# Kernel tuning notes

Hardware: AMD Instinct MI355X
Metric: run time of the kernel (lower is better)

Reference implementation:

```python
import jax, jax.numpy as jnp
import numpy as np

V, D, T, B, MS, WIN, EOS = 10000, 256, 128, 8, 4, 1, 4
S = MS + 1          # decoder segment length (y_input0 + MAX_SEGMENT tokens)
HRATE = 0.1
LOGINF = 1e6


def setup_inputs() -> dict:
    key = jax.random.key(0)
    ks = jax.random.split(key, 17)
    s = lambda i, shape: (jax.random.normal(ks[i], shape, jnp.float32) * 0.05)
    return dict(
        x_ids=jax.random.randint(ks[0], (B, T + 2 * WIN), 0, V),
        lens=jnp.full((B,), T, dtype=jnp.int32),
        emb=s(1, (V, D)),
        y_start=s(2, (1, D)),
        cell_Wi=s(3, (4 * D, D)), cell_Wh=s(4, (4 * D, D)), cell_b=s(5, (4 * D,)),
        yin0_W=s(6, (D, D)), yin0_b=s(7, (D,)),
        hlin_W=s(8, (2 * D, D)), hlin_b=s(9, (2 * D,)),
        l0_Wi=s(10, (4 * D, D)), l0_Wh=s(11, (4 * D, D)), l0_b=s(12, (4 * D,)),
        l1_Wi=s(13, (4 * D, D)), l1_Wh=s(14, (4 * D, D)), l1_b=s(15, (4 * D,)),
        out_b=s(16, (V,)),
    )


def _cell(x, h, c, Wi, Wh, b):
    # torch LSTM gate order: i, f, g, o
    g = x @ Wi.T + h @ Wh.T + b
    i, f, gg, o = jnp.split(g, 4, axis=-1)
    c2 = jax.nn.sigmoid(f) * c + jax.nn.sigmoid(i) * jnp.tanh(gg)
    return jax.nn.sigmoid(o) * jnp.tanh(c2), c2


def reference(x_ids, lens, emb, y_start, cell_Wi, cell_Wh, cell_b,
              yin0_W, yin0_b, hlin_W, hlin_b,
              l0_Wi, l0_Wh, l0_b, l1_Wi, l1_Wh, l1_b, out_b):
    y = x_ids[:, WIN:-WIN]                     # [B, T] target ids
    x = emb[y]                                 # [B, T, D]

    # --- encoder LSTMCell scan over j_start (state persists across schedule) ---
    seq = jnp.concatenate(
        [jnp.broadcast_to(y_start, (B, D))[None], jnp.transpose(x, (1, 0, 2))[:-1]], 0)  # [T,B,D]
    z = jnp.zeros((B, D), x.dtype)
    def enc_step(carry, xt):
        h, c = carry
        h2, c2 = _cell(xt, h, c, cell_Wi, cell_Wh, cell_b)
        return (h2, c2), h2
    _, h_seq = jax.lax.scan(enc_step, (z, z), seq)        # [T, B, D]

    drop_h = HRATE * h_seq
    y_in0 = drop_h @ yin0_W.T + yin0_b                    # [T, B, D]
    h0_all = jnp.tanh(drop_h @ hlin_W.T + hlin_b).reshape(T, B, 2, D)  # per-layer init h

    # --- build decoder inputs [T, B, S, D]: (y_input0, x[j_start:j_start+MS]) ---
    xp = jnp.pad(x, ((0, 0), (0, MS), (0, 0)))            # zero-pad time (causal => pads don't affect valid outputs)
    pos = jnp.arange(T)[:, None] + jnp.arange(MS)[None, :]           # [T, MS]
    seg_x = jnp.transpose(xp[:, pos], (1, 0, 2, 3))       # [T, B, MS, D]
    seg = jnp.concatenate([y_in0[:, :, None, :], seg_x], axis=2)     # [T, B, S, D]

    # --- 2-layer LSTM decoder, vmapped over j_start ---
    def decode(seg_t, h_init):                            # seg_t [B,S,D], h_init [B,2,D]
        def step(carry, xt):
            (h0, c0), (h1, c1) = carry
            h0n, c0n = _cell(xt, h0, c0, l0_Wi, l0_Wh, l0_b)
            h1n, c1n = _cell(h0n, h1, c1, l1_Wi, l1_Wh, l1_b)
            return ((h0n, c0n), (h1n, c1n)), h1n
        init = ((h_init[:, 0], z), (h_init[:, 1], z))
        _, hs = jax.lax.scan(step, init, jnp.transpose(seg_t, (1, 0, 2)))
        return jnp.transpose(hs, (1, 0, 2))               # [B, S, D]
    dec_h = jax.vmap(decode)(seg, h0_all)                 # [T, B, S, D]

    # --- tied output projection + log-softmax (only needed gathers kept) ---
    logits = jnp.einsum('tbsd,vd->tbsv', dec_h, emb) + out_b         # [T,B,S,V]
    logZ = jax.nn.logsumexp(logits, axis=-1)                          # [T,B,S]

    tgt = jnp.transpose(y[:, jnp.clip(pos, 0, T - 1)], (1, 0, 2))     # [T,B,MS]
    tgt_lp = jnp.take_along_axis(logits[:, :, :MS, :], tgt[..., None], axis=3)[..., 0] \
             - logZ[:, :, :MS]                                        # [T,B,MS]
    pmask = (pos < T)[:, None, :]
    cum = jnp.cumsum(jnp.where(pmask, tgt_lp, 0.0), axis=2)           # [T,B,MS]
    eos_lp = logits[:, :, 1:, EOS] - logZ[:, :, 1:]                   # [T,B,MS]

    kmask = (jnp.arange(T)[:, None] + jnp.arange(1, MS + 1)[None, :]) <= T   # [T,MS]
    body = jnp.where(kmask[:, None, :], cum + eos_lp, -LOGINF)        # [T,B,MS]
    logpy = jnp.concatenate([jnp.full((T, 1, B), -LOGINF, body.dtype),
                             jnp.transpose(body, (0, 2, 1))], axis=1)  # [T, MS+1, B]

    # --- alpha forward DP: alpha[j] = logsumexp_L alpha[j-L] + logpy[j-L][L] ---
    jj = jnp.arange(1, T + 1)[:, None]
    ii = jnp.arange(MS)[None, :]
    sstart = jj - MS + ii                                             # [T,MS]
    LPG = jnp.where((sstart >= 0)[..., None],
                    logpy[jnp.clip(sstart, 0), jnp.broadcast_to(MS - ii, (T, MS))],
                    -LOGINF)                                          # [T,MS,B]

    Apad0 = jnp.full((MS + T + 1, B), -LOGINF, logpy.dtype).at[MS].set(0.0)
    def dp_step(Apad, args):
        j, lpg = args
        win = jax.lax.dynamic_slice(Apad, (j, 0), (MS, B))            # alpha[j-MS .. j-1]
        aj = jax.nn.logsumexp(win + lpg, axis=0)
        return jax.lax.dynamic_update_slice(Apad, aj[None], (MS + j, 0)), None
    Apad, _ = jax.lax.scan(dp_step, Apad0, (jnp.arange(1, T + 1), LPG))
    alpha = Apad[MS:]                                                 # [T+1, B]

    ret = -jnp.sum(alpha[lens, jnp.arange(B)]) / jnp.sum(lens).astype(alpha.dtype)
    return ret
```

## Files before the change

### kernel.cpp

```cpp
#include <hip/hip_runtime.h>

#define V_ 10000
#define D_ 256
#define T_ 128
#define B_ 8
#define MS_ 4
#define S_ 5
#define EOS_ 4

typedef unsigned short b16_t;
typedef __attribute__((ext_vector_type(8))) short s16x8;
typedef __attribute__((ext_vector_type(8))) unsigned short u16x8;
typedef __attribute__((ext_vector_type(4))) float f32x4;
typedef __attribute__((ext_vector_type(2))) _Float16 h16x2;

__device__ inline b16_t f2bf(float f) {
  union { float f; unsigned u; } v; v.f = f;
  unsigned r = v.u + 0x7FFFu + ((v.u >> 16) & 1u);
  return (b16_t)(r >> 16);
}
__device__ inline float bf2f(b16_t h) {
  union { unsigned u; float f; } v; v.u = ((unsigned)h) << 16; return v.f;
}
__device__ inline float sigm_(float x) { return 1.0f / (1.0f + __expf(-x)); }
__device__ inline float tanh_(float x) { return 2.0f / (1.0f + __expf(-2.0f * x)) - 1.0f; }
__device__ inline h16x2 bch(unsigned u) { return __builtin_bit_cast(h16x2, u); }
__device__ inline unsigned pkh(float a, float b) {
  h16x2 v; v.x = (_Float16)a; v.y = (_Float16)b;
  return __builtin_bit_cast(unsigned, v);
}

#if __has_builtin(__builtin_amdgcn_fdot2)
#define FDOT2(a, b, c) __builtin_amdgcn_fdot2((a), (b), (c), false)
#else
#define FDOT2(a, b, c) ((c) + (float)(a).x * (float)(b).x + (float)(a).y * (float)(b).y)
#endif

__device__ inline float qswap1(float x) {
  return __builtin_bit_cast(float, __builtin_amdgcn_update_dpp(
      0, __builtin_bit_cast(int, x), 0xB1, 0xF, 0xF, true));
}

__device__ inline void cvt4(const float* __restrict__ s, b16_t* __restrict__ d) {
  float4 v = *(const float4*)s;
  ushort4 o = { f2bf(v.x), f2bf(v.y), f2bf(v.z), f2bf(v.w) };
  *(ushort4*)d = o;
}

__global__ void k_prep(const float* __restrict__ emb, const float* __restrict__ cWi,
                       const float* __restrict__ y0W, const float* __restrict__ hlW,
                       const float* __restrict__ l0Wi, const float* __restrict__ l0Wh,
                       const float* __restrict__ l1Wi, const float* __restrict__ l1Wh,
                       const float* __restrict__ cWh, const int* __restrict__ x_ids,
                       const float* __restrict__ y_st,
                       b16_t* __restrict__ emb_bf, b16_t* __restrict__ cWi_bf,
                       b16_t* __restrict__ y0W_bf, b16_t* __restrict__ hlW_bf,
                       b16_t* __restrict__ l0Wi_bf, b16_t* __restrict__ l0Wh_bf,
                       b16_t* __restrict__ Wcat_bf, unsigned* __restrict__ Whf,
                       b16_t* __restrict__ seq_bf, b16_t* __restrict__ seg_bf) {
  for (long i = (long)blockIdx.x * blockDim.x + threadIdx.x; i < 1410048L;
       i += (long)gridDim.x * blockDim.x) {
    if (i < 640000L) { cvt4(emb + i * 4, emb_bf + i * 4); }
    else if (i < 705536L) { long j = i - 640000L; cvt4(cWi + j * 4, cWi_bf + j * 4); }
    else if (i < 721920L) { long j = i - 705536L; cvt4(y0W + j * 4, y0W_bf + j * 4); }
    else if (i < 754688L) { long j = i - 721920L; cvt4(hlW + j * 4, hlW_bf + j * 4); }
    else if (i < 820224L) { long j = i - 754688L; cvt4(l0Wi + j * 4, l0Wi_bf + j * 4); }
    else if (i < 885760L) { long j = i - 820224L; cvt4(l0Wh + j * 4, l0Wh_bf + j * 4); }
    else if (i < 1016832L) {
      long j = (i - 885760L) * 4;
      long n = j >> 9; int k = (int)(j & 511);
      const float* src = (k < 256) ? (l1Wi + n * 256 + k) : (l1Wh + n * 256 + (k - 256));
      cvt4(src, Wcat_bf + j);
    } else if (i < 1082368L) {
      long j = i - 1016832L;
      float4 v = *(const float4*)(cWh + j * 4);
      Whf[2 * j] = pkh(v.x, v.y);
      Whf[2 * j + 1] = pkh(v.z, v.w);
    } else if (i < 1147904L) {
      long j = i - 1082368L;
      int m = (int)(j >> 6), c = (int)(j & 63) * 4;
      int t = m >> 3, b = m & 7;
      const float* src = (t == 0) ? (y_st + c)
                                  : (emb + (size_t)x_ids[b * (T_ + 2) + t] * D_ + c);
      cvt4(src, seq_bf + (size_t)m * D_ + c);
    } else {
      long j = i - 1147904L;
      int r = (int)(j >> 6), c = (int)(j & 63) * 4;
      int p = r >> 2, s = 1 + (r & 3);
      int t = p >> 3, b = p & 7;
      int tt = t + s - 1;
      int ps = r + (r >> 2) + 1;
      if (tt < T_) {
        int tok = x_ids[b * (T_ + 2) + tt + 1];
        cvt4(emb + (size_t)tok * D_ + c, seg_bf + (size_t)ps * 256 + c);
      } else {
        ushort4 z = {0, 0, 0, 0};
        *(ushort4*)(seg_bf + (size_t)ps * 256 + c) = z;
      }
    }
  }
}

__global__ __launch_bounds__(256) void k_gemm(const b16_t* __restrict__ A, int lda,
                                              const b16_t* __restrict__ Bw,
                                              const float* __restrict__ bias,
                                              float* __restrict__ C, int ldc) {
  __shared__ b16_t As[64][264];
  __shared__ b16_t Bs[64][264];
  int tid = threadIdx.x;
  int rowBase = blockIdx.x * 64, colBase = blockIdx.y * 64;
  for (int i = tid; i < 64 * 32; i += 256) {
    int r = i >> 5, c = (i & 31) * 8;
    *(u16x8*)&As[r][c] = *(const u16x8*)(A + (size_t)(rowBase + r) * lda + c);
    *(u16x8*)&Bs[r][c] = *(const u16x8*)(Bw + (size_t)(colBase + r) * 256 + c);
  }
  __syncthreads();
  int w = tid >> 6, l = tid & 63, lr = l & 15, kg = l >> 4;
  f32x4 acc[4] = {{0.f,0.f,0.f,0.f},{0.f,0.f,0.f,0.f},{0.f,0.f,0.f,0.f},{0.f,0.f,0.f,0.f}};
  for (int kk = 0; kk < 8; ++kk) {
    s16x8 a = *(const s16x8*)&As[w * 16 + lr][kk * 32 + kg * 8];
#pragma unroll
    for (int f = 0; f < 4; ++f) {
      s16x8 b = *(const s16x8*)&Bs[f * 16 + lr][kk * 32 + kg * 8];
      acc[f] = __builtin_amdgcn_mfma_f32_16x16x32_bf16(a, b, acc[f], 0, 0, 0);
    }
  }
#pragma unroll
  for (int f = 0; f < 4; ++f) {
#pragma unroll
    for (int r = 0; r < 4; ++r) {
      int m = rowBase + w * 16 + kg * 4 + r;
      int n = colBase + f * 16 + lr;
      C[(size_t)m * ldc + n] = acc[f][r] + bias[n];
    }
  }
}

#define ENC_CH4(i0)                                                            \
  do {                                                                         \
    uint4 a0 = hp[i0], a1 = hp[i0 + 1], a2 = hp[i0 + 2], a3 = hp[i0 + 3];      \
    s0 = FDOT2(bch(a0.x), bch(wv[4 * (i0) + 0]), s0);                          \
    s1 = FDOT2(bch(a0.y), bch(wv[4 * (i0) + 1]), s1);                          \
    s0 = FDOT2(bch(a0.z), bch(wv[4 * (i0) + 2]), s0);                          \
    s1 = FDOT2(bch(a0.w), bch(wv[4 * (i0) + 3]), s1);                          \
    s0 = FDOT2(bch(a1.x), bch(wv[4 * (i0) + 4]), s0);                          \
    s1 = FDOT2(bch(a1.y), bch(wv[4 * (i0) + 5]), s1);                          \
    s0 = FDOT2(bch(a1.z), bch(wv[4 * (i0) + 6]), s0);                          \
    s1 = FDOT2(bch(a1.w), bch(wv[4 * (i0) + 7]), s1);                          \
    s0 = FDOT2(bch(a2.x), bch(wv[4 * (i0) + 8]), s0);                          \
    s1 = FDOT2(bch(a2.y), bch(wv[4 * (i0) + 9]), s1);                          \
    s0 = FDOT2(bch(a2.z), bch(wv[4 * (i0) + 10]), s0);                         \
    s1 = FDOT2(bch(a2.w), bch(wv[4 * (i0) + 11]), s1);                         \
    s0 = FDOT2(bch(a3.x), bch(wv[4 * (i0) + 12]), s0);                         \
    s1 = FDOT2(bch(a3.y), bch(wv[4 * (i0) + 13]), s1);                         \
    s0 = FDOT2(bch(a3.z), bch(wv[4 * (i0) + 14]), s0);                         \
    s1 = FDOT2(bch(a3.w), bch(wv[4 * (i0) + 15]), s1);                         \
  } while (0)

struct EncS { unsigned hbuf[128]; float gl[256]; };
struct GemS { b16_t As[64][264]; b16_t Bs[64][264]; };

__global__ __launch_bounds__(512, 2) void k_enc_x0(
    const unsigned* __restrict__ Whf,
    const float* __restrict__ encX,
    unsigned* __restrict__ hglob,
    b16_t* __restrict__ droph,
    const b16_t* __restrict__ seg_bf, const b16_t* __restrict__ l0Wi_bf,
    const float* __restrict__ l0b, float* __restrict__ X0) {
  __shared__ union { EncS e; GemS g; } sm;
  int tid = threadIdx.x;
  if (blockIdx.x < 32) {
    int b = blockIdx.x & 7, q = blockIdx.x >> 3;
    int r = tid >> 1, ch = tid & 1;
    int growr = ((r >> 6) << 8) + q * 64 + (r & 63);
    unsigned wv[64];
    {
      const uint4* wp = (const uint4*)(Whf + (size_t)growr * 128 + ch * 64);
#pragma unroll
      for (int i = 0; i < 16; ++i) {
        uint4 v = wp[i];
        wv[4*i] = v.x; wv[4*i+1] = v.y; wv[4*i+2] = v.z; wv[4*i+3] = v.w;
      }
    }
#pragma unroll
    for (int i = 0; i < 64; ++i) asm volatile("" : "+v"(wv[i]));
    if (tid < 128) sm.e.hbuf[tid] = 0;
    float c = 0.f;
    float ex = encX[(size_t)b * 1024 + growr];
    __syncthreads();
#pragma unroll 1
    for (int t = 0; t < 128; ++t) {
      const uint4* hp = (const uint4*)&sm.e.hbuf[ch * 64];
      float s0 = 0.f, s1 = 0.f;
      ENC_CH4(0);
      __builtin_amdgcn_sched_barrier(0);
      ENC_CH4(4);
      __builtin_amdgcn_sched_barrier(0);
      ENC_CH4(8);
      __builtin_amdgcn_sched_barrier(0);
      ENC_CH4(12);
      float sum = s0 + s1;
      sum += qswap1(sum);
      if (ch == 0) sm.e.gl[r] = sum + ex;
      __syncthreads();
      if (tid < 64) {
        float gi = sm.e.gl[tid], gf = sm.e.gl[64 + tid];
        float gg = sm.e.gl[128 + tid], go = sm.e.gl[192 + tid];
        float c2 = sigm_(gf) * c + sigm_(gi) * tanh_(gg);
        float h2 = sigm_(go) * tanh_(c2);
        c = c2;
        float hnb = qswap1(h2);
        if ((tid & 1) == 0) {
          unsigned pk = pkh(h2, hnb) | 0x00010001u;
          sm.e.hbuf[q * 32 + (tid >> 1)] = pk;
          if (t < 127)
            __hip_atomic_store(&hglob[(((size_t)t * 8 + b) * 4 + q) * 32 + (tid >> 1)],
                               pk, __ATOMIC_RELAXED, __HIP_MEMORY_SCOPE_AGENT);
        }
        droph[((size_t)t * 8 + b) * 256 + q * 64 + tid] = f2bf(0.1f * h2);
      }
      if (t < 127) {
        if (tid >= 64 && tid < 160) {
          int idx = tid - 64;
          int ro = idx >> 5;
          int rq = ro + (ro >= q);
          int dw = idx & 31;
          unsigned* src = &hglob[(((size_t)t * 8 + b) * 4 + rq) * 32 + dw];
          unsigned v;
          do {
            v = __hip_atomic_load(src, __ATOMIC_RELAXED, __HIP_MEMORY_SCOPE_AGENT);
          } while (v == 0u);
          sm.e.hbuf[rq * 32 + dw] = v;
        }
        ex = encX[((size_t)(t + 1) * 8 + b) * 1024 + growr];
        __syncthreads();
      }
    }
  } else {
    int bx2 = blockIdx.x - 32;
    int rb = (bx2 & 63) * 64;
    int colBase = (bx2 >> 6) * 64;
    if (tid < 256) {
      for (int i = tid; i < 64 * 32; i += 256) {
        int r = i >> 5, cc = (i & 31) * 8;
        int jj = rb + r, ps = jj + (jj >> 2) + 1;
        *(u16x8*)&sm.g.As[r][cc] = *(const u16x8*)(seg_bf + (size_t)ps * 256 + cc);
        *(u16x8*)&sm.g.Bs[r][cc] = *(const u16x8*)(l0Wi_bf + (size_t)(colBase + r) * 256 + cc);
      }
    }
    __syncthreads();
    if (tid < 256) {
      int w = tid >> 6, l = tid & 63, lr = l & 15, kg = l >> 4;
      f32x4 acc[4] = {{0.f,0.f,0.f,0.f},{0.f,0.f,0.f,0.f},{0.f,0.f,0.f,0.f},{0.f,0.f,0.f,0.f}};
      for (int kk = 0; kk < 8; ++kk) {
        s16x8 a = *(const s16x8*)&sm.g.As[w * 16 + lr][kk * 32 + kg * 8];
#pragma unroll
        for (int f = 0; f < 4; ++f) {
          s16x8 b = *(const s16x8*)&sm.g.Bs[f * 16 + lr][kk * 32 + kg * 8];
          acc[f] = __builtin_amdgcn_mfma_f32_16x16x32_bf16(a, b, acc[f], 0, 0, 0);
        }
      }
#pragma unroll
      for (int f = 0; f < 4; ++f) {
#pragma unroll
        for (int r = 0; r < 4; ++r) {
          int jj = rb + w * 16 + kg * 4 + r;
          int ps = jj + (jj >> 2) + 1;
          int n = colBase + f * 16 + lr;
          X0[(size_t)ps * 1024 + n] = acc[f][r] + l0b[n];
        }
      }
    }
  }
}

__global__ __launch_bounds__(256) void k_proj(
    const b16_t* __restrict__ droph, const b16_t* __restrict__ y0W_bf,
    const float* __restrict__ y0b, const b16_t* __restrict__ hlW_bf,
    const float* __restrict__ hlb, b16_t* __restrict__ seg_bf,
    b16_t* __restrict__ hcat) {
  __shared__ b16_t As[64][264];
  __shared__ b16_t Bs[64][264];
  int bx = blockIdx.x, by = blockIdx.y;
  const b16_t* Bw; const float* bias; int colBase, mode;
  if (by < 4) { Bw = y0W_bf; bias = y0b; colBase = by * 64; mode = 0; }
  else { Bw = hlW_bf; bias = hlb; colBase = (by - 4) * 64; mode = 1; }
  int rowBase = bx * 64;
  int tid = threadIdx.x;
  for (int i = tid; i < 64 * 32; i += 256) {
    int r = i >> 5, c = (i & 31) * 8;
    *(u16x8*)&As[r][c] = *(const u16x8*)(droph + (size_t)(rowBase + r) * 256 + c);
    *(u16x8*)&Bs[r][c] = *(const u16x8*)(Bw + (size_t)(colBase + r) * 256 + c);
  }
  __syncthreads();
  int w = tid >> 6, l = tid & 63, lr = l & 15, kg = l >> 4;
  f32x4 acc[4] = {{0.f,0.f,0.f,0.f},{0.f,0.f,0.f,0.f},{0.f,0.f,0.f,0.f},{0.f,0.f,0.f,0.f}};
  for (int kk = 0; kk < 8; ++kk) {
    s16x8 a = *(const s16x8*)&As[w * 16 + lr][kk * 32 + kg * 8];
#pragma unroll
    for (int f = 0; f < 4; ++f) {
      s16x8 b = *(const s16x8*)&Bs[f * 16 + lr][kk * 32 + kg * 8];
      acc[f] = __builtin_amdgcn_mfma_f32_16x16x32_bf16(a, b, acc[f], 0, 0, 0);
    }
  }
#pragma unroll
  for (int f = 0; f < 4; ++f) {
#pragma unroll
    for (int r = 0; r < 4; ++r) {
      int m = rowBase + w * 16 + kg * 4 + r;
      int n = colBase + f * 16 + lr;
      float v = acc[f][r] + bias[n];
      if (mode == 0) seg_bf[(size_t)m * 1280 + n] = f2bf(v);
      else hcat[(size_t)m * 512 + n] = f2bf(tanh_(v));
    }
  }
}

__global__ __launch_bounds__(512) void k_dec2(
    b16_t* __restrict__ hcat,
    const b16_t* __restrict__ l0Wh_bf,
    const b16_t* __restrict__ Wcat_bf,
    const float* __restrict__ X0,
    const float* __restrict__ l1b,
    float* __restrict__ c0, float* __restrict__ c1,
    b16_t* __restrict__ dec_out, int s) {
  __shared__ b16_t A0s[16][264];
  __shared__ b16_t A1s[16][520];
  int tid = threadIdx.x;
  int R0 = blockIdx.x * 16;
  for (int i = tid; i < 16 * 32; i += 512) {
    int r = i >> 5, cc = (i & 31) * 8;
    *(u16x8*)&A0s[r][cc] = *(const u16x8*)(hcat + (size_t)(R0 + r) * 512 + cc);
    *(u16x8*)&A1s[r][256 + cc] = *(const u16x8*)(hcat + (size_t)(R0 + r) * 512 + 256 + cc);
  }
  __syncthreads();
  int w = tid >> 6, l = tid & 63, lr = l & 15, kg = l >> 4;
  {
    s16x8 af[8];
#pragma unroll
    for (int kk = 0; kk < 8; ++kk)
      af[kk] = *(const s16x8*)&A0s[lr][kk * 32 + kg * 8];
    f32x4 acc[4][2];
#pragma unroll
    for (int g = 0; g < 4; ++g)
#pragma unroll
      for (int ct = 0; ct < 2; ++ct) acc[g][ct] = f32x4{0.f, 0.f, 0.f, 0.f};
#pragma unroll
    for (int g = 0; g < 4; ++g)
#pragma unroll
      for (int ct = 0; ct < 2; ++ct) {
        int n = g * 256 + w * 32 + ct * 16 + lr;
        const b16_t* bp = l0Wh_bf + (size_t)n * 256 + kg * 8;
#pragma unroll
        for (int kk = 0; kk < 8; ++kk)
          acc[g][ct] = __builtin_amdgcn_mfma_f32_16x16x32_bf16(
              af[kk], *(const s16x8*)(bp + kk * 32), acc[g][ct], 0, 0, 0);
      }
#pragma unroll
    for (int ct = 0; ct < 2; ++ct)
#pragma unroll
      for (int r = 0; r < 4; ++r) {
        int row = kg * 4 + r, p = R0 + row, d = w * 32 + ct * 16 + lr;
        const float* xp = X0 + ((size_t)p * 5 + s) * 1024;
        float gi = acc[0][ct][r] + xp[d],       gf = acc[1][ct][r] + xp[256 + d];
        float gg = acc[2][ct][r] + xp[512 + d], go = acc[3][ct][r] + xp[768 + d];
        float cc0 = c0[(size_t)p * 256 + d];
        float c2 = sigm_(gf) * cc0 + sigm_(gi) * tanh_(gg);
        float h2 = sigm_(go) * tanh_(c2);
        c0[(size_t)p * 256 + d] = c2;
        b16_t hb = f2bf(h2);
        A1s[row][d] = hb;
        hcat[(size_t)p * 512 + d] = hb;
      }
  }
  __syncthreads();
  {
    s16x8 a1[16];
#pragma unroll
    for (int kk = 0; kk < 16; ++kk)
      a1[kk] = *(const s16x8*)&A1s[lr][kk * 32 + kg * 8];
    f32x4 acc[4][2];
#pragma unroll
    for (int g = 0; g < 4; ++g)
#pragma unroll
      for (int ct = 0; ct < 2; ++ct) acc[g][ct] = f32x4{0.f, 0.f, 0.f, 0.f};
#pragma unroll
    for (int g = 0; g < 4; ++g)
#pragma unroll
      for (int ct = 0; ct < 2; ++ct) {
        int n = g * 256 + w * 32 + ct * 16 + lr;
        const b16_t* bp = Wcat_bf + (size_t)n * 512 + kg * 8;
#pragma unroll
        for (int kk = 0; kk < 16; ++kk)
          acc[g][ct] = __builtin_amdgcn_mfma_f32_16x16x32_bf16(
              a1[kk], *(const s16x8*)(bp + kk * 32), acc[g][ct], 0, 0, 0);
      }
#pragma unroll
    for (int ct = 0; ct < 2; ++ct)
#pragma unroll
      for (int r = 0; r < 4; ++r) {
        int row = kg * 4 + r, p = R0 + row, d = w * 32 + ct * 16 + lr;
        float gi = acc[0][ct][r] + l1b[d],       gf = acc[1][ct][r] + l1b[256 + d];
        float gg = acc[2][ct][r] + l1b[512 + d], go = acc[3][ct][r] + l1b[768 + d];
        float cc1 = c1[(size_t)p * 256 + d];
        float c2 = sigm_(gf) * cc1 + sigm_(gi) * tanh_(gg);
        float h2 = sigm_(go) * tanh_(c2);
        c1[(size_t)p * 256 + d] = c2;
        b16_t hb = f2bf(h2);
        hcat[(size_t)p * 512 + 256 + d] = hb;
        dec_out[((size_t)p * 5 + s) * 256 + d] = hb;
      }
  }
}

__global__ __launch_bounds__(512) void k_logits(const b16_t* __restrict__ Abf,
                                                const b16_t* __restrict__ emb_bf,
                                                const float* __restrict__ out_b,
                                                float* __restrict__ sumexp) {
  __shared__ b16_t Bs[64][264];
  int tid = threadIdx.x;
  int rowBase = blockIdx.x * 256;
  int w = tid >> 6, l = tid & 63, lr = l & 15, kg = l >> 4;
  s16x8 af[2][8];
#pragma unroll
  for (int mt = 0; mt < 2; ++mt) {
    const b16_t* arow = Abf + (size_t)(rowBase + mt * 128 + w * 16 + lr) * 256;
#pragma unroll
    for (int kk = 0; kk < 8; ++kk) af[mt][kk] = *(const s16x8*)(arow + kk * 32 + kg * 8);
  }
  float runsum[2][4] = {{0.f,0.f,0.f,0.f},{0.f,0.f,0.f,0.f}};
  int t0 = blockIdx.y * 12, t1 = (t0 + 12 < 157) ? (t0 + 12) : 157;
  for (int tile = t0; tile < t1; ++tile) {
    int colBase = tile * 64;
    __syncthreads();
    for (int i = tid; i < 64 * 32; i += 512) {
      int r = i >> 5, cc = (i & 31) * 8;
      int vrow = colBase + r;
      u16x8 bv = {0, 0, 0, 0, 0, 0, 0, 0};
      if (vrow < V_) bv = *(const u16x8*)(emb_bf + (size_t)vrow * D_ + cc);
      *(u16x8*)&Bs[r][cc] = bv;
    }
    __syncthreads();
    f32x4 acc[2][4];
#pragma unroll
    for (int mt = 0; mt < 2; ++mt)
#pragma unroll
      for (int f = 0; f < 4; ++f) acc[mt][f] = f32x4{0.f, 0.f, 0.f, 0.f};
#pragma unroll
    for (int kk = 0; kk < 8; ++kk) {
#pragma unroll
      for (int f = 0; f < 4; ++f) {
        s16x8 b = *(const s16x8*)&Bs[f * 16 + lr][kk * 32 + kg * 8];
#pragma unroll
        for (int mt = 0; mt < 2; ++mt)
          acc[mt][f] = __builtin_amdgcn_mfma_f32_16x16x32_bf16(af[mt][kk], b, acc[mt][f], 0, 0, 0);
      }
    }
#pragma unroll
    for (int f = 0; f < 4; ++f) {
      int n = colBase + f * 16 + lr;
      if (n < V_) {
        float ob = out_b[n];
#pragma unroll
        for (int mt = 0; mt < 2; ++mt)
#pragma unroll
          for (int r = 0; r < 4; ++r) runsum[mt][r] += __expf(acc[mt][f][r] + ob);
      }
    }
  }
#pragma unroll
  for (int mt = 0; mt < 2; ++mt)
#pragma unroll
    for (int r = 0; r < 4; ++r) {
      float rs = runsum[mt][r];
      rs += __shfl_xor(rs, 1, 64);
      rs += __shfl_xor(rs, 2, 64);
      rs += __shfl_xor(rs, 4, 64);
      rs += __shfl_xor(rs, 8, 64);
      if (lr == 0)
        atomicAdd(&sumexp[rowBase + mt * 128 + w * 16 + kg * 4 + r], rs);
    }
}

__global__ void k_extract(const b16_t* __restrict__ dec_h, const b16_t* __restrict__ emb_bf,
                          const float* __restrict__ out_b, const int* __restrict__ x_ids,
                          float* __restrict__ tl, float* __restrict__ el) {
  int p = blockIdx.x, lane = threadIdx.x;
  int t = p >> 3, b = p & 7;
  for (int s = 0; s < S_; ++s) {
    const b16_t* hr = dec_h + ((size_t)p * S_ + s) * D_;
    float hv[4];
#pragma unroll
    for (int j = 0; j < 4; ++j) hv[j] = bf2f(hr[lane * 4 + j]);
    if (s < MS_) {
      int pos = t + s; if (pos > T_ - 1) pos = T_ - 1;
      int tok = x_ids[b * (T_ + 2) + pos + 1];
      const b16_t* er = emb_bf + (size_t)tok * D_;
      float ps = 0.f;
#pragma unroll
      for (int j = 0; j < 4; ++j) ps += hv[j] * bf2f(er[lane * 4 + j]);
      for (int m = 1; m < 64; m <<= 1) ps += __shfl_xor(ps, m, 64);
      if (lane == 0) tl[p * MS_ + s] = ps + out_b[tok];
    }
    if (s >= 1) {
      const b16_t* er = emb_bf + (size_t)EOS_ * D_;
      float ps = 0.f;
#pragma unroll
      for (int j = 0; j < 4; ++j) ps += hv[j] * bf2f(er[lane * 4 + j]);
      for (int m = 1; m < 64; m <<= 1) ps += __shfl_xor(ps, m, 64);
      if (lane == 0) el[p * MS_ + (s - 1)] = ps + out_b[EOS_];
    }
  }
}

__global__ __launch_bounds__(256) void k_final(const float* __restrict__ sumexp,
                                               const float* __restrict__ tl,
                                               const float* __restrict__ el,
                                               const int* __restrict__ lens,
                                               float* __restrict__ out) {
  __shared__ float logpy[T_][S_][B_];
  __shared__ float alpha[T_ + 1][B_];
  int tid = threadIdx.x;
  for (int p = tid; p < T_ * B_; p += 256) {
    int t = p >> 3, b = p & 7;
    float lz[S_];
#pragma unroll
    for (int s = 0; s < S_; ++s) lz[s] = __logf(sumexp[p * S_ + s]);
    float cum = 0.f, cums[MS_];
#pragma unroll
    for (int s = 0; s < MS_; ++s) {
      float tlp = tl[p * MS_ + s] - lz[s];
      if (t + s < T_) cum += tlp;
      cums[s] = cum;
    }
#pragma unroll
    for (int k = 1; k <= MS_; ++k) {
      float bv = -1000000.0f;
      if (t + k <= T_) bv = cums[k - 1] + (el[p * MS_ + (k - 1)] - lz[k]);
      logpy[t][k][b] = bv;
    }
  }
  __syncthreads();
  if (tid < B_) {
    int b = tid;
    alpha[0][b] = 0.f;
    for (int j = 1; j <= T_; ++j) {
      float vs[MS_], vmax = -1e30f;
#pragma unroll
      for (int k = 1; k <= MS_; ++k) {
        float vv = -2000000.0f;
        if (j - k >= 0) vv = alpha[j - k][b] + logpy[j - k][k][b];
        vs[k - 1] = vv;
        if (vv > vmax) vmax = vv;
      }
      float ssum = 0.f;
#pragma unroll
      for (int k = 0; k < MS_; ++k) ssum += __expf(vs[k] - vmax);
      alpha[j][b] = vmax + __logf(ssum);
    }
  }
  __syncthreads();
  if (tid == 0) {
    float num = 0.f, den = 0.f;
    for (int b = 0; b < B_; ++b) { num += alpha[lens[b]][b]; den += (float)lens[b]; }
    out[0] = -num / den;
  }
}

extern "C" void kernel_launch(void* const* d_in, const int* in_sizes, int n_in,
                              void* d_out, int out_size, void* d_ws, size_t ws_size,
                              hipStream_t stream) {
  const int* x_ids   = (const int*)d_in[0];
  const int* lens    = (const int*)d_in[1];
  const float* emb   = (const float*)d_in[2];
  const float* y_st  = (const float*)d_in[3];
  const float* cWi   = (const float*)d_in[4];
  const float* cWh   = (const float*)d_in[5];
  const float* cb    = (const float*)d_in[6];
  const float* y0W   = (const float*)d_in[7];
  const float* y0b   = (const float*)d_in[8];
  const float* hlW   = (const float*)d_in[9];
  const float* hlb   = (const float*)d_in[10];
  const float* l0Wi  = (const float*)d_in[11];
  const float* l0Wh  = (const float*)d_in[12];
  const float* l0b   = (const float*)d_in[13];
  const float* l1Wi  = (const float*)d_in[14];
  const float* l1Wh  = (const float*)d_in[15];
  const float* l1b   = (const float*)d_in[16];
  const float* outb  = (const float*)d_in[17];
  float* out = (float*)d_out;
  (void)in_sizes; (void)n_in; (void)out_size; (void)ws_size;

  char* ws = (char*)d_ws;
  size_t cur = 0;
  auto alloc = [&](size_t bytes) { size_t o = cur; cur += (bytes + 255) & ~(size_t)255; return o; };
  b16_t* emb_bf    = (b16_t*)(ws + alloc((size_t)V_ * D_ * 2));
  b16_t* cWi_bf    = (b16_t*)(ws + alloc(1024 * 256 * 2));
  b16_t* y0W_bf    = (b16_t*)(ws + alloc(256 * 256 * 2));
  b16_t* hlW_bf    = (b16_t*)(ws + alloc(512 * 256 * 2));
  b16_t* l0Wi_bf   = (b16_t*)(ws + alloc(1024 * 256 * 2));
  b16_t* l0Wh_bf   = (b16_t*)(ws + alloc(1024 * 256 * 2));
  b16_t* Wcat_bf   = (b16_t*)(ws + alloc(1024 * 512 * 2));
  unsigned* Whf    = (unsigned*)(ws + alloc(1024 * 128 * 4));
  b16_t* seq_bf    = (b16_t*)(ws + alloc(1024 * 256 * 2));
  float* encX      = (float*)(ws + alloc((size_t)1024 * 1024 * 4));
  b16_t* droph_bf  = (b16_t*)(ws + alloc(1024 * 256 * 2));
  b16_t* hcat      = (b16_t*)(ws + alloc(1024 * 512 * 2));
  b16_t* seg_bf    = (b16_t*)(ws + alloc((size_t)5120 * 256 * 2));
  float* X0        = (float*)(ws + alloc((size_t)5120 * 1024 * 4));
  float* c0        = (float*)(ws + alloc((size_t)2 * 1024 * 256 * 4));
  float* c1        = c0 + 1024 * 256;
  b16_t* dec_h_bf  = (b16_t*)(ws + alloc((size_t)5120 * 256 * 2));
  float* sumexp    = (float*)(ws + alloc(5120 * 4));
  unsigned* hglob  = (unsigned*)(ws + alloc((size_t)128 * 8 * 4 * 32 * 4));
  float* tl        = (float*)(ws + alloc(1024 * MS_ * 4));
  float* el        = (float*)(ws + alloc(1024 * MS_ * 4));

  hipMemsetAsync(sumexp, 0, 20480 + 524288, stream);
  hipMemsetAsync(c0, 0, (size_t)2 * 1024 * 256 * 4, stream);

  k_prep<<<1024, 256, 0, stream>>>(emb, cWi, y0W, hlW, l0Wi, l0Wh, l1Wi, l1Wh, cWh,
                                   x_ids, y_st,
                                   emb_bf, cWi_bf, y0W_bf, hlW_bf, l0Wi_bf, l0Wh_bf,
                                   Wcat_bf, Whf, seq_bf, seg_bf);

  k_gemm<<<dim3(16, 16), 256, 0, stream>>>(seq_bf, 256, cWi_bf, cb, encX, 1024);
  k_enc_x0<<<1056, 512, 0, stream>>>(Whf, encX, hglob, droph_bf,
                                     seg_bf, l0Wi_bf, l0b, X0);

  k_proj<<<dim3(16, 12), 256, 0, stream>>>(droph_bf, y0W_bf, y0b, hlW_bf, hlb,
                                           seg_bf, hcat);
  k_gemm<<<dim3(16, 16), 256, 0, stream>>>(seg_bf, 1280, l0Wi_bf, l0b, X0, 5120);

  for (int s = 0; s < S_; ++s)
    k_dec2<<<64, 512, 0, stream>>>(hcat, l0Wh_bf, Wcat_bf, X0, l1b, c0, c1, dec_h_bf, s);

  k_logits<<<dim3(20, 14), 512, 0, stream>>>(dec_h_bf, emb_bf, outb, sumexp);
  k_extract<<<1024, 64, 0, stream>>>(dec_h_bf, emb_bf, outb, x_ids, tl, el);
  k_final<<<1, 256, 0, stream>>>(sumexp, tl, el, lens, out);
}
```

Before: 575.5 us.

## Fuse encoder input GEMM into recurrent kernel with flag polling; halve logits row tile

The separate encoder input-projection GEMM launch is removed. Its tiles are computed by extra blocks inside the encoder recurrence kernel, which publish each value with the low bit forced set (zero acts as a not-ready flag). The recurrent blocks spin on these values, so the recurrence can start before the whole projection finishes, and encX is zeroed beforehand. Separately, the logits kernel now handles 128 rows per block instead of 256, doubling the grid for more parallelism at the cost of reloading B tiles more often. The fused path relies on the GEMM blocks being scheduled alongside the spinning blocks, and setting the low bit perturbs the fp32 values slightly.

New measurement: 565.4 us. No clear change (-1.8%).

```diff
diff --git a/kernel.cpp b/kernel.cpp
--- a/kernel.cpp
+++ b/kernel.cpp
@@ -39,6 +39,15 @@
 __device__ inline float qswap1(float x) {
   return __builtin_bit_cast(float, __builtin_amdgcn_update_dpp(
       0, __builtin_bit_cast(int, x), 0xB1, 0xF, 0xF, true));
+}
+
+__device__ inline float poll_f(const float* p) {
+  union { unsigned u; float f; } v;
+  do {
+    v.u = __hip_atomic_load((const unsigned*)p, __ATOMIC_RELAXED,
+                            __HIP_MEMORY_SCOPE_AGENT);
+  } while (v.u == 0u);
+  return v.f;
 }
 
 __device__ inline void cvt4(const float* __restrict__ s, b16_t* __restrict__ d) {
@@ -162,9 +171,11 @@
 
 __global__ __launch_bounds__(512, 2) void k_enc_x0(
     const unsigned* __restrict__ Whf,
-    const float* __restrict__ encX,
+    float* __restrict__ encX,
     unsigned* __restrict__ hglob,
     b16_t* __restrict__ droph,
+    const b16_t* __restrict__ seq_bf, const b16_t* __restrict__ cWi_bf,
+    const float* __restrict__ cb,
     const b16_t* __restrict__ seg_bf, const b16_t* __restrict__ l0Wi_bf,
     const float* __restrict__ l0b, float* __restrict__ X0) {
   __shared__ union { EncS e; GemS g; } sm;
@@ -186,8 +197,9 @@
     for (int i = 0; i < 64; ++i) asm volatile("" : "+v"(wv[i]));
     if (tid < 128) sm.e.hbuf[tid] = 0;
     float c = 0.f;
-    float ex = encX[(size_t)b * 1024 + growr];
+    float ex0 = poll_f(&encX[(size_t)b * 1024 + growr]);
     __syncthreads();
+    float ex = ex0;
 #pragma unroll 1
     for (int t = 0; t < 128; ++t) {
       const uint4* hp = (const uint4*)&sm.e.hbuf[ch * 64];
@@ -232,20 +244,28 @@
           } while (v == 0u);
           sm.e.hbuf[rq * 32 + dw] = v;
         }
-        ex = encX[((size_t)(t + 1) * 8 + b) * 1024 + growr];
+        ex = poll_f(&encX[((size_t)(t + 1) * 8 + b) * 1024 + growr]);
         __syncthreads();
       }
     }
   } else {
     int bx2 = blockIdx.x - 32;
-    int rb = (bx2 & 63) * 64;
-    int colBase = (bx2 >> 6) * 64;
+    const b16_t* Ab; const b16_t* Bw; const float* bias; int rb, colBase, isX0;
+    if (bx2 < 256) {
+      rb = (bx2 >> 4) * 64; colBase = (bx2 & 15) * 64;
+      Ab = seq_bf; Bw = cWi_bf; bias = cb; isX0 = 0;
+    } else {
+      int b3 = bx2 - 256;
+      rb = (b3 & 63) * 64; colBase = (b3 >> 6) * 64;
+      Ab = seg_bf; Bw = l0Wi_bf; bias = l0b; isX0 = 1;
+    }
     if (tid < 256) {
       for (int i = tid; i < 64 * 32; i += 256) {
         int r = i >> 5, cc = (i & 31) * 8;
-        int jj = rb + r, ps = jj + (jj >> 2) + 1;
-        *(u16x8*)&sm.g.As[r][cc] = *(const u16x8*)(seg_bf + (size_t)ps * 256 + cc);
-        *(u16x8*)&sm.g.Bs[r][cc] = *(const u16x8*)(l0Wi_bf + (size_t)(colBase + r) * 256 + cc);
+        int jj = rb + r;
+        int ar = isX0 ? (jj + (jj >> 2) + 1) : jj;
+        *(u16x8*)&sm.g.As[r][cc] = *(const u16x8*)(Ab + (size_t)ar * 256 + cc);
+        *(u16x8*)&sm.g.Bs[r][cc] = *(const u16x8*)(Bw + (size_t)(colBase + r) * 256 + cc);
       }
     }
     __syncthreads();
@@ -265,9 +285,17 @@
 #pragma unroll
         for (int r = 0; r < 4; ++r) {
           int jj = rb + w * 16 + kg * 4 + r;
-          int ps = jj + (jj >> 2) + 1;
           int n = colBase + f * 16 + lr;
-          X0[(size_t)ps * 1024 + n] = acc[f][r] + l0b[n];
+          if (isX0) {
+            int ps = jj + (jj >> 2) + 1;
+            X0[(size_t)ps * 1024 + n] = acc[f][r] + bias[n];
+          } else {
+            union { float f; unsigned u; } vv;
+            vv.f = acc[f][r] + bias[n];
+            vv.u |= 1u;
+            __hip_atomic_store((unsigned*)&encX[(size_t)jj * 1024 + n], vv.u,
+                               __ATOMIC_RELAXED, __HIP_MEMORY_SCOPE_AGENT);
+          }
         }
       }
     }
@@ -419,16 +447,15 @@
                                                 float* __restrict__ sumexp) {
   __shared__ b16_t Bs[64][264];
   int tid = threadIdx.x;
-  int rowBase = blockIdx.x * 256;
+  int rowBase = blockIdx.x * 128;
   int w = tid >> 6, l = tid & 63, lr = l & 15, kg = l >> 4;
-  s16x8 af[2][8];
-#pragma unroll
-  for (int mt = 0; mt < 2; ++mt) {
-    const b16_t* arow = Abf + (size_t)(rowBase + mt * 128 + w * 16 + lr) * 256;
-#pragma unroll
-    for (int kk = 0; kk < 8; ++kk) af[mt][kk] = *(const s16x8*)(arow + kk * 32 + kg * 8);
-  }
-  float runsum[2][4] = {{0.f,0.f,0.f,0.f},{0.f,0.f,0.f,0.f}};
+  s16x8 af[8];
+  {
+    const b16_t* arow = Abf + (size_t)(rowBase + w * 16 + lr) * 256;
+#pragma unroll
+    for (int kk = 0; kk < 8; ++kk) af[kk] = *(const s16x8*)(arow + kk * 32 + kg * 8);
+  }
+  float runsum[4] = {0.f, 0.f, 0.f, 0.f};
   int t0 = blockIdx.y * 12, t1 = (t0 + 12 < 157) ? (t0 + 12) : 157;
   for (int tile = t0; tile < t1; ++tile) {
     int colBase = tile * 64;
@@ -441,19 +468,13 @@
       *(u16x8*)&Bs[r][cc] = bv;
     }
     __syncthreads();
-    f32x4 acc[2][4];
-#pragma unroll
-    for (int mt = 0; mt < 2; ++mt)
-#pragma unroll
-      for (int f = 0; f < 4; ++f) acc[mt][f] = f32x4{0.f, 0.f, 0.f, 0.f};
+    f32x4 acc[4] = {{0.f,0.f,0.f,0.f},{0.f,0.f,0.f,0.f},{0.f,0.f,0.f,0.f},{0.f,0.f,0.f,0.f}};
 #pragma unroll
     for (int kk = 0; kk < 8; ++kk) {
 #pragma unroll
       for (int f = 0; f < 4; ++f) {
         s16x8 b = *(const s16x8*)&Bs[f * 16 + lr][kk * 32 + kg * 8];
-#pragma unroll
-        for (int mt = 0; mt < 2; ++mt)
-          acc[mt][f] = __builtin_amdgcn_mfma_f32_16x16x32_bf16(af[mt][kk], b, acc[mt][f], 0, 0, 0);
+        acc[f] = __builtin_amdgcn_mfma_f32_16x16x32_bf16(af[kk], b, acc[f], 0, 0, 0);
       }
     }
 #pragma unroll
@@ -462,24 +483,19 @@
       if (n < V_) {
         float ob = out_b[n];
 #pragma unroll
-        for (int mt = 0; mt < 2; ++mt)
-#pragma unroll
-          for (int r = 0; r < 4; ++r) runsum[mt][r] += __expf(acc[mt][f][r] + ob);
-      }
-    }
-  }
-#pragma unroll
-  for (int mt = 0; mt < 2; ++mt)
-#pragma unroll
-    for (int r = 0; r < 4; ++r) {
-      float rs = runsum[mt][r];
-      rs += __shfl_xor(rs, 1, 64);
-      rs += __shfl_xor(rs, 2, 64);
-      rs += __shfl_xor(rs, 4, 64);
-      rs += __shfl_xor(rs, 8, 64);
-      if (lr == 0)
-        atomicAdd(&sumexp[rowBase + mt * 128 + w * 16 + kg * 4 + r], rs);
-    }
+        for (int r = 0; r < 4; ++r) runsum[r] += __expf(acc[f][r] + ob);
+      }
+    }
+  }
+#pragma unroll
+  for (int r = 0; r < 4; ++r) {
+    float rs = runsum[r];
+    rs += __shfl_xor(rs, 1, 64);
+    rs += __shfl_xor(rs, 2, 64);
+    rs += __shfl_xor(rs, 4, 64);
+    rs += __shfl_xor(rs, 8, 64);
+    if (lr == 0) atomicAdd(&sumexp[rowBase + w * 16 + kg * 4 + r], rs);
+  }
 }
 
 __global__ void k_extract(const b16_t* __restrict__ dec_h, const b16_t* __restrict__ emb_bf,
@@ -617,6 +633,7 @@
   float* el        = (float*)(ws + alloc(1024 * MS_ * 4));
 
   hipMemsetAsync(sumexp, 0, 20480 + 524288, stream);
+  hipMemsetAsync(encX, 0, (size_t)1024 * 1024 * 4, stream);
   hipMemsetAsync(c0, 0, (size_t)2 * 1024 * 256 * 4, stream);
 
   k_prep<<<1024, 256, 0, stream>>>(emb, cWi, y0W, hlW, l0Wi, l0Wh, l1Wi, l1Wh, cWh,
@@ -624,8 +641,8 @@
                                    emb_bf, cWi_bf, y0W_bf, hlW_bf, l0Wi_bf, l0Wh_bf,
                                    Wcat_bf, Whf, seq_bf, seg_bf);
 
-  k_gemm<<<dim3(16, 16), 256, 0, stream>>>(seq_bf, 256, cWi_bf, cb, encX, 1024);
-  k_enc_x0<<<1056, 512, 0, stream>>>(Whf, encX, hglob, droph_bf,
+  k_enc_x0<<<1312, 512, 0, stream>>>(Whf, encX, hglob, droph_bf,
+                                     seq_bf, cWi_bf, cb,
                                      seg_bf, l0Wi_bf, l0b, X0);
 
   k_proj<<<dim3(16, 12), 256, 0, stream>>>(droph_bf, y0W_bf, y0b, hlW_bf, hlb,
@@ -635,7 +652,7 @@
   for (int s = 0; s < S_; ++s)
     k_dec2<<<64, 512, 0, stream>>>(hcat, l0Wh_bf, Wcat_bf, X0, l1b, c0, c1, dec_h_bf, s);
 
-  k_logits<<<dim3(20, 14), 512, 0, stream>>>(dec_h_bf, emb_bf, outb, sumexp);
+  k_logits<<<dim3(40, 14), 512, 0, stream>>>(dec_h_bf, emb_bf, outb, sumexp);
   k_extract<<<1024, 64, 0, stream>>>(dec_h_bf, emb_bf, outb, x_ids, tl, el);
   k_final<<<1, 256, 0, stream>>>(sumexp, tl, el, lens, out);
 }
```
